# Kernel tuning notes

Hardware: AMD Instinct MI355X
Metric: run time of the kernel (lower is better)

## Reference

```python
import jax, jax.numpy as jnp
import numpy as np

# dims: batch, d_features(m), n_subsets, sub_size(k=ceil(m/n)), heads, d_k, d_v, conv kernel, d_out
B, M, N, K, H, DK, DV, KER, D = 512, 4096, 64, 64, 8, 32, 4, 3, 4096
DOUT_PER = D // N  # d_out_per_subset = 64
EPS_LN = 1e-5      # torch nn.LayerNorm default eps


def setup_inputs() -> dict:
    key = jax.random.key(0)
    ks = jax.random.split(key, 8)
    s = 0.02  # xavier-like scale
    return {
        "features": jax.random.normal(ks[0], (B, M), dtype=jnp.float32),
        # per-head permutation of the m feature indices (f_shuffle(m, h, seeds))
        "shuffled_index": jnp.argsort(jax.random.uniform(ks[1], (H, M)), axis=1).astype(jnp.int32),
        "gamma": jnp.ones((M,), jnp.float32),
        "beta": jnp.zeros((M,), jnp.float32),
        "W_q": (jax.random.normal(ks[2], (H * DK, K)) * s).astype(jnp.float32),   # Linear(k, h*d_k)
        "W_k": (jax.random.normal(ks[3], (H, DK, K)) * s).astype(jnp.float32),    # grouped Conv1d(h, h*d_k, kernel=k, stride=k)
        "W_v1": (jax.random.normal(ks[4], (H, DV, KER)) * s).astype(jnp.float32), # grouped Conv1d(h, h*d_v, kernel)
        "W_v2": (jax.random.normal(ks[5], (H, DV)) * s).astype(jnp.float32),      # grouped Conv1d(h*d_v, h, 1)
        "W_fc": (jax.random.normal(ks[6], (DOUT_PER, H * K)) * s).astype(jnp.float32),
    }


def reference(features, shuffled_index, gamma, beta, W_q, W_k, W_v1, W_v2, W_fc):
    b = features.shape[0]
    # LayerNorm over m (query path only)
    mu = features.mean(-1, keepdims=True)
    var = ((features - mu) ** 2).mean(-1, keepdims=True)
    q_in = (features - mu) / jnp.sqrt(var + EPS_LN) * gamma + beta

    # shuffled gather: [b, H, M]  (k*n == m here so k_pad/q_pad are no-ops)
    sf = features[:, shuffled_index]

    # query: [b, n, k] -> Linear(k, h*d_k) -> [b, H, N, DK]
    q = jnp.einsum('bnk,ek->bne', q_in.reshape(b, N, K), W_q)
    q = q.reshape(b, N, H, DK).transpose(0, 2, 1, 3)

    # key: grouped conv kernel=stride=k == per-subset contraction -> [b, H, DK, N]
    kf = sf.reshape(b, H, N, K)
    key_ = jnp.einsum('bhnk,hdk->bhdn', kf, W_k)

    # value: [b, N, H, K], right-pad by KER-1, depthwise conv -> relu -> 1x1 conv -> +residual
    v = kf.transpose(0, 2, 1, 3)  # [b, N, H, K]
    vp = jnp.pad(v, ((0, 0), (0, 0), (0, 0), (0, KER - 1)))
    win = jnp.stack([vp[..., t:t + K] for t in range(KER)], axis=-1)  # [b,N,H,K,KER]
    v1 = jnp.einsum('bnhpt,hdt->bnhdp', win, W_v1)
    v2 = jnp.einsum('bnhdp,hd->bnhp', jax.nn.relu(v1), W_v2)
    v = (v2 + v).transpose(0, 2, 1, 3)  # [b, H, N, K]

    # scaled dot-product attention, temperature = sqrt(m)
    attn = jax.nn.softmax(jnp.einsum('bhqd,bhdk->bhqk', q, key_) / jnp.sqrt(jnp.float32(M)), axis=-1)
    out = jnp.einsum('bhqk,bhks->bhqs', attn, v)           # [b, H, N, K]
    out = out.transpose(0, 2, 1, 3).reshape(b, N, H * K)   # [b, N, H*K]
    out = jnp.einsum('bnf,of->bno', out, W_fc).reshape(b, N * DOUT_PER)
    return out, attn.reshape(b * H, N, N)
```

## Files before the change

### kernel.cpp

```cpp
#include <hip/hip_runtime.h>

typedef __bf16 v8bf __attribute__((ext_vector_type(8)));
typedef __bf16 v4bf __attribute__((ext_vector_type(4)));
typedef __bf16 v2bf __attribute__((ext_vector_type(2)));
typedef float  v4f  __attribute__((ext_vector_type(4)));

namespace {

constexpr int kB = 512, kM = 4096, kH = 8;

constexpr size_t WS_QIN = 0;
constexpr size_t WS_O   = (size_t)4 << 20;
constexpr size_t WS_WQ  = WS_O + (size_t)32768 * 512 * 2;
constexpr size_t WS_WK  = WS_WQ + 32768;
constexpr size_t WS_WFC = WS_WK + 32768;


__global__ __launch_bounds__(256) void k0_weights(
    const float* __restrict__ Wq, const float* __restrict__ Wk,
    const float* __restrict__ Wfc,
    __bf16* __restrict__ wq, __bf16* __restrict__ wk, __bf16* __restrict__ wfc) {
  int i = blockIdx.x * 256 + threadIdx.x;
  if (i < 16384) {
    int e = i >> 6, k = i & 63;
    int dst = ((e >> 4) * 2 + (k >> 5)) * 512 + (e & 15) * 32 + (k & 31);
    wq[dst] = (__bf16)(Wq[i] * 0.015625f);
  } else if (i < 32768) {
    int j = i - 16384;
    int e = j >> 6, k = j & 63;
    int dst = ((e >> 4) * 2 + (k >> 5)) * 512 + (e & 15) * 32 + (k & 31);
    wk[dst] = (__bf16)Wk[j];
  } else {
    int j = i - 32768;
    int o = j >> 9, f = j & 511;
    int dst = ((o >> 4) * 16 + (f >> 5)) * 512 + (o & 15) * 32 + (f & 31);
    wfc[dst] = (__bf16)Wfc[j];
  }
}

__global__ __launch_bounds__(256) void k1_ln(
    const float* __restrict__ feat, const float* __restrict__ gamma,
    const float* __restrict__ beta, __bf16* __restrict__ qin) {
  __shared__ float red[4];
  const int b = blockIdx.x, t = threadIdx.x, lane = t & 63, wv = t >> 6;
  const float* frow = feat + (size_t)b * kM;
  float xs[16];
  float s = 0.f;
#pragma unroll
  for (int j = 0; j < 16; ++j) { float x = frow[t + j * 256]; xs[j] = x; s += x; }
#pragma unroll
  for (int o = 32; o > 0; o >>= 1) s += __shfl_xor(s, o);
  if (lane == 0) red[wv] = s;
  __syncthreads();
  const float mu = (red[0] + red[1] + red[2] + red[3]) * (1.f / kM);
  float v = 0.f;
#pragma unroll
  for (int j = 0; j < 16; ++j) { float d = xs[j] - mu; v += d * d; }
#pragma unroll
  for (int o = 32; o > 0; o >>= 1) v += __shfl_xor(v, o);
  __syncthreads();
  if (lane == 0) red[wv] = v;
  __syncthreads();
  const float var  = (red[0] + red[1] + red[2] + red[3]) * (1.f / kM);
  const float rstd = rsqrtf(var + 1e-5f);
#pragma unroll
  for (int j = 0; j < 16; ++j) {
    int m = t + j * 256;
    int n = m >> 6, k = m & 63;
    int dst = ((n >> 4) * 2 + (k >> 5)) * 512 + (n & 15) * 32 + (k & 31);
    qin[(size_t)b * kM + dst] = (__bf16)((xs[j] - mu) * rstd * gamma[m] + beta[m]);
  }
}

__global__ __launch_bounds__(256, 4) void k2_attn(
    const float* __restrict__ feat, const int* __restrict__ sidx,
    const __bf16* __restrict__ qin, const __bf16* __restrict__ wq,
    const __bf16* __restrict__ wk, const float* __restrict__ Wv1,
    const float* __restrict__ Wv2, __bf16* __restrict__ o_ws,
    float* __restrict__ out) {
  __shared__ __align__(16) __bf16 smem[18432];
  __bf16* s_feat = smem;
  __bf16* s_kf   = smem + 4096;
  __bf16* s_q    = smem + 8704;
  __bf16* s_K    = smem + 11264;
  __bf16* s_vT   = smem + 13824;
  __bf16* s_sc   = smem + 4096;

  const int b = blockIdx.x, h = blockIdx.y;
  const int t = threadIdx.x, w = t >> 6, lid = t & 63;
  const int quad = lid >> 4, l16 = lid & 15;

  const float*  frow  = feat + (size_t)b * kM;
  const int*    idxh  = sidx + h * kM;
  const __bf16* qin_b = qin + (size_t)b * kM;
  float* attn_out = out + (size_t)kB * kM + ((size_t)(b * kH + h)) * 4096;

  int idxr[16];
#pragma unroll
  for (int j = 0; j < 16; ++j) idxr[j] = idxh[t + j * 256];

  {
    const float4* frow4 = reinterpret_cast<const float4*>(frow);
#pragma unroll
    for (int j = 0; j < 4; ++j) {
      int i4 = t + j * 256;
      float4 f = frow4[i4];
      v4bf o4;
      o4[0] = (__bf16)f.x; o4[1] = (__bf16)f.y; o4[2] = (__bf16)f.z; o4[3] = (__bf16)f.w;
      *(v4bf*)(s_feat + 4 * i4) = o4;
    }
  }

  if (t < 64) {
    v8bf z = {};
    *(v8bf*)(s_kf + t * 72 + 64) = z;
  }

  v4f dq0 = {0.f, 0.f, 0.f, 0.f}, dq1 = {0.f, 0.f, 0.f, 0.f};
#pragma unroll
  for (int kt = 0; kt < 2; ++kt) {
    v8bf a  = *(const v8bf*)(qin_b + (2 * w + kt) * 512 + l16 * 32 + 8 * quad);
    v8bf b0 = *(const v8bf*)(wq + (size_t)(4 * h + kt) * 512 + l16 * 32 + 8 * quad);
    v8bf b1 = *(const v8bf*)(wq + (size_t)(4 * h + 2 + kt) * 512 + l16 * 32 + 8 * quad);
    dq0 = __builtin_amdgcn_mfma_f32_16x16x32_bf16(a, b0, dq0, 0, 0, 0);
    dq1 = __builtin_amdgcn_mfma_f32_16x16x32_bf16(a, b1, dq1, 0, 0, 0);
  }
#pragma unroll
  for (int r = 0; r < 4; ++r) {
    s_q[(16 * w + 4 * quad + r) * 40 + l16]      = (__bf16)dq0[r];
    s_q[(16 * w + 4 * quad + r) * 40 + 16 + l16] = (__bf16)dq1[r];
  }

  __syncthreads();

#pragma unroll
  for (int j = 0; j < 16; ++j) {
    int i = t + j * 256;
    s_kf[(i >> 6) * 72 + (i & 63)] = s_feat[idxr[j]];
  }

  __syncthreads();

  {
    v4f dk0 = {0.f, 0.f, 0.f, 0.f}, dk1 = {0.f, 0.f, 0.f, 0.f};
#pragma unroll
    for (int kt = 0; kt < 2; ++kt) {
      v8bf a  = *(const v8bf*)(s_kf + (16 * w + l16) * 72 + 32 * kt + 8 * quad);
      v8bf b0 = *(const v8bf*)(wk + (size_t)(4 * h + kt) * 512 + l16 * 32 + 8 * quad);
      v8bf b1 = *(const v8bf*)(wk + (size_t)(4 * h + 2 + kt) * 512 + l16 * 32 + 8 * quad);
      dk0 = __builtin_amdgcn_mfma_f32_16x16x32_bf16(a, b0, dk0, 0, 0, 0);
      dk1 = __builtin_amdgcn_mfma_f32_16x16x32_bf16(a, b1, dk1, 0, 0, 0);
    }
#pragma unroll
    for (int r = 0; r < 4; ++r) {
      s_K[(16 * w + 4 * quad + r) * 40 + l16]      = (__bf16)dk0[r];
      s_K[(16 * w + 4 * quad + r) * 40 + 16 + l16] = (__bf16)dk1[r];
    }
  }

  {
    const int n = t & 63, p0 = (t >> 6) * 16;
    float w1[4][3], w2[4];
#pragma unroll
    for (int d = 0; d < 4; ++d) {
#pragma unroll
      for (int c = 0; c < 3; ++c) w1[d][c] = Wv1[(h * 4 + d) * 3 + c];
      w2[d] = Wv2[h * 4 + d];
    }
    v8bf xa = *(const v8bf*)(s_kf + n * 72 + p0);
    v8bf xb = *(const v8bf*)(s_kf + n * 72 + p0 + 8);
    v2bf xc = *(const v2bf*)(s_kf + n * 72 + p0 + 16);
    float x[18];
#pragma unroll
    for (int c = 0; c < 8; ++c) { x[c] = (float)xa[c]; x[c + 8] = (float)xb[c]; }
    x[16] = (float)xc[0]; x[17] = (float)xc[1];
#pragma unroll
    for (int pp = 0; pp < 16; ++pp) {
      float acc = x[pp];
#pragma unroll
      for (int d = 0; d < 4; ++d) {
        float v1 = fmaf(x[pp + 2], w1[d][2], fmaf(x[pp + 1], w1[d][1], x[pp] * w1[d][0]));
        acc = fmaf(fmaxf(v1, 0.f), w2[d], acc);
      }
      s_vT[(p0 + pp) * 72 + n] = (__bf16)acc;
    }
  }

  __syncthreads();

  {
    v4f ds[4] = {{0.f, 0.f, 0.f, 0.f}, {0.f, 0.f, 0.f, 0.f},
                 {0.f, 0.f, 0.f, 0.f}, {0.f, 0.f, 0.f, 0.f}};
    v8bf a = *(const v8bf*)(s_q + (16 * w + l16) * 40 + 8 * quad);
#pragma unroll
    for (int nt = 0; nt < 4; ++nt) {
      v8bf bb = *(const v8bf*)(s_K + (16 * nt + l16) * 40 + 8 * quad);
      ds[nt] = __builtin_amdgcn_mfma_f32_16x16x32_bf16(a, bb, ds[nt], 0, 0, 0);
    }
#pragma unroll
    for (int nt = 0; nt < 4; ++nt)
#pragma unroll
      for (int r = 0; r < 4; ++r)
        s_sc[(16 * w + 4 * quad + r) * 72 + 16 * nt + l16] = (__bf16)ds[nt][r];
  }

#pragma unroll
  for (int rr = 0; rr < 4; ++rr) {
    const int row = 16 * w + 4 * rr + quad;
    v4bf pv = *(const v4bf*)(s_sc + row * 72 + 4 * l16);
    float e0 = (float)pv[0], e1 = (float)pv[1], e2 = (float)pv[2], e3 = (float)pv[3];
    float mx = fmaxf(fmaxf(e0, e1), fmaxf(e2, e3));
#pragma unroll
    for (int mk = 8; mk > 0; mk >>= 1) mx = fmaxf(mx, __shfl_xor(mx, mk));
    e0 = __expf(e0 - mx); e1 = __expf(e1 - mx);
    e2 = __expf(e2 - mx); e3 = __expf(e3 - mx);
    float ssum = e0 + e1 + e2 + e3;
#pragma unroll
    for (int mk = 8; mk > 0; mk >>= 1) ssum += __shfl_xor(ssum, mk);
    const float inv = 1.0f / ssum;
    e0 *= inv; e1 *= inv; e2 *= inv; e3 *= inv;
    *(float4*)(attn_out + row * 64 + 4 * l16) = make_float4(e0, e1, e2, e3);
    v4bf st;
    st[0] = (__bf16)e0; st[1] = (__bf16)e1; st[2] = (__bf16)e2; st[3] = (__bf16)e3;
    *(v4bf*)(s_sc + row * 72 + 4 * l16) = st;
  }

  v4f dO[4] = {{0.f, 0.f, 0.f, 0.f}, {0.f, 0.f, 0.f, 0.f},
               {0.f, 0.f, 0.f, 0.f}, {0.f, 0.f, 0.f, 0.f}};
#pragma unroll
  for (int kt = 0; kt < 2; ++kt) {
    v8bf a = *(const v8bf*)(s_sc + (16 * w + l16) * 72 + 32 * kt + 8 * quad);
#pragma unroll
    for (int st = 0; st < 4; ++st) {
      v8bf bb = *(const v8bf*)(s_vT + (16 * st + l16) * 72 + 32 * kt + 8 * quad);
      dO[st] = __builtin_amdgcn_mfma_f32_16x16x32_bf16(a, bb, dO[st], 0, 0, 0);
    }
  }

  __bf16* obase = o_ws + ((size_t)(b * 4 + w) * 16 + h * 2) * 512;
#pragma unroll
  for (int st = 0; st < 4; ++st)
#pragma unroll
    for (int r = 0; r < 4; ++r)
      obase[(st >> 1) * 512 + (4 * quad + r) * 32 + (st & 1) * 16 + l16] = (__bf16)dO[st][r];
}

__global__ __launch_bounds__(256, 4) void k3_fc(
    const __bf16* __restrict__ o_ws, const __bf16* __restrict__ wfc,
    float* __restrict__ out) {
  const int t = threadIdx.x, w = t >> 6, lid = t & 63;
  const int quad = lid >> 4, l16 = lid & 15;
  const size_t row0 = (size_t)blockIdx.x * 64 + 16 * w;
  const __bf16* abase = o_ws + (size_t)(blockIdx.x * 4 + w) * 16 * 512;
  v4f d[4] = {{0.f, 0.f, 0.f, 0.f}, {0.f, 0.f, 0.f, 0.f},
              {0.f, 0.f, 0.f, 0.f}, {0.f, 0.f, 0.f, 0.f}};
#pragma unroll 4
  for (int kt = 0; kt < 16; ++kt) {
    v8bf a = *(const v8bf*)(abase + kt * 512 + l16 * 32 + 8 * quad);
#pragma unroll
    for (int nt = 0; nt < 4; ++nt) {
      v8bf bb = *(const v8bf*)(wfc + (size_t)(nt * 16 + kt) * 512 + l16 * 32 + 8 * quad);
      d[nt] = __builtin_amdgcn_mfma_f32_16x16x32_bf16(a, bb, d[nt], 0, 0, 0);
    }
  }
#pragma unroll
  for (int nt = 0; nt < 4; ++nt)
#pragma unroll
    for (int r = 0; r < 4; ++r)
      out[(row0 + 4 * quad + r) * 64 + 16 * nt + l16] = d[nt][r];
}

}

extern "C" void kernel_launch(void* const* d_in, const int* in_sizes, int n_in,
                              void* d_out, int out_size, void* d_ws, size_t ws_size,
                              hipStream_t stream) {
  (void)in_sizes; (void)n_in; (void)out_size; (void)ws_size;
  const float* features = (const float*)d_in[0];
  const int*   sidx     = (const int*)d_in[1];
  const float* gamma    = (const float*)d_in[2];
  const float* beta     = (const float*)d_in[3];
  const float* Wq       = (const float*)d_in[4];
  const float* Wk       = (const float*)d_in[5];
  const float* Wv1      = (const float*)d_in[6];
  const float* Wv2      = (const float*)d_in[7];
  const float* Wfc      = (const float*)d_in[8];
  float* out = (float*)d_out;

  char* ws = (char*)d_ws;
  __bf16* ws_qin = (__bf16*)(ws + WS_QIN);
  __bf16* ws_o   = (__bf16*)(ws + WS_O);
  __bf16* ws_wq  = (__bf16*)(ws + WS_WQ);
  __bf16* ws_wk  = (__bf16*)(ws + WS_WK);
  __bf16* ws_wfc = (__bf16*)(ws + WS_WFC);

  hipLaunchKernelGGL(k0_weights, dim3(256), dim3(256), 0, stream,
                     Wq, Wk, Wfc, ws_wq, ws_wk, ws_wfc);
  hipLaunchKernelGGL(k1_ln, dim3(kB), dim3(256), 0, stream,
                     features, gamma, beta, ws_qin);
  hipLaunchKernelGGL(k2_attn, dim3(kB, kH), dim3(256), 0, stream,
                     features, sidx, ws_qin, ws_wq, ws_wk, Wv1, Wv2, ws_o, out);
  hipLaunchKernelGGL(k3_fc, dim3(kB), dim3(256), 0, stream,
                     ws_o, ws_wfc, out);
}
```

Baseline: 150.2 us.

## Fold W_q and W_k into a per-head combined matrix and keep softmax in registers

Precomputes a per-head 64x64 matrix Wq^T·Wk (with the temperature scale) in a small weight kernel. The attention kernel then computes qin·Wqk once and contracts it with the shuffled features, instead of building separate Q and K projections. Softmax now runs directly on the MFMA accumulators instead of going through an LDS round trip, and attention probabilities are written with nontemporal stores. LDS use drops, allowing occupancy to rise from 4 to 5 blocks, at the cost of an extra tiny serial precompute launch and a different bf16 rounding path.

```diff
diff --git a/kernel.cpp b/kernel.cpp
--- a/kernel.cpp
+++ b/kernel.cpp
@@ -11,30 +11,41 @@
 
 constexpr size_t WS_QIN = 0;
 constexpr size_t WS_O   = (size_t)4 << 20;
-constexpr size_t WS_WQ  = WS_O + (size_t)32768 * 512 * 2;
-constexpr size_t WS_WK  = WS_WQ + 32768;
-constexpr size_t WS_WFC = WS_WK + 32768;
-
-
-__global__ __launch_bounds__(256) void k0_weights(
+constexpr size_t WS_WFC = WS_O + (size_t)32768 * 512 * 2;
+constexpr size_t WS_WQK = WS_WFC + 65536;
+
+
+__global__ __launch_bounds__(256) void k0_wfc(
+    const float* __restrict__ Wfc, __bf16* __restrict__ wfc) {
+  int j = blockIdx.x * 256 + threadIdx.x;
+  int o = j >> 9, f = j & 511;
+  int dst = ((o >> 4) * 16 + (f >> 5)) * 512 + (o & 15) * 32 + (f & 31);
+  wfc[dst] = (__bf16)Wfc[j];
+}
+
+__global__ __launch_bounds__(256) void k0b_wqk(
     const float* __restrict__ Wq, const float* __restrict__ Wk,
-    const float* __restrict__ Wfc,
-    __bf16* __restrict__ wq, __bf16* __restrict__ wk, __bf16* __restrict__ wfc) {
-  int i = blockIdx.x * 256 + threadIdx.x;
-  if (i < 16384) {
-    int e = i >> 6, k = i & 63;
-    int dst = ((e >> 4) * 2 + (k >> 5)) * 512 + (e & 15) * 32 + (k & 31);
-    wq[dst] = (__bf16)(Wq[i] * 0.015625f);
-  } else if (i < 32768) {
-    int j = i - 16384;
-    int e = j >> 6, k = j & 63;
-    int dst = ((e >> 4) * 2 + (k >> 5)) * 512 + (e & 15) * 32 + (k & 31);
-    wk[dst] = (__bf16)Wk[j];
-  } else {
-    int j = i - 32768;
-    int o = j >> 9, f = j & 511;
-    int dst = ((o >> 4) * 16 + (f >> 5)) * 512 + (o & 15) * 32 + (f & 31);
-    wfc[dst] = (__bf16)Wfc[j];
+    __bf16* __restrict__ wqk) {
+  __shared__ float sq[2048], sk[2048];
+  const int h = blockIdx.x, t = threadIdx.x;
+#pragma unroll
+  for (int j = 0; j < 8; ++j) {
+    sq[t + j * 256] = Wq[h * 2048 + t + j * 256] * 0.015625f;
+    sk[t + j * 256] = Wk[h * 2048 + t + j * 256];
+  }
+  __syncthreads();
+  const int kp = t >> 2, kbase = (t & 3) * 16;
+  float wkr[32];
+#pragma unroll
+  for (int d = 0; d < 32; ++d) wkr[d] = sk[d * 64 + kp];
+#pragma unroll
+  for (int j = 0; j < 16; ++j) {
+    int k = kbase + j;
+    float acc = 0.f;
+#pragma unroll
+    for (int d = 0; d < 32; ++d) acc = fmaf(sq[d * 64 + k], wkr[d], acc);
+    int dst = h * 4096 + ((kp >> 4) * 2 + (k >> 5)) * 512 + (kp & 15) * 32 + (k & 31);
+    wqk[dst] = (__bf16)acc;
   }
 }
 
@@ -72,19 +83,15 @@
   }
 }
 
-__global__ __launch_bounds__(256, 4) void k2_attn(
+__global__ __launch_bounds__(256, 5) void k2_attn(
     const float* __restrict__ feat, const int* __restrict__ sidx,
-    const __bf16* __restrict__ qin, const __bf16* __restrict__ wq,
-    const __bf16* __restrict__ wk, const float* __restrict__ Wv1,
-    const float* __restrict__ Wv2, __bf16* __restrict__ o_ws,
-    float* __restrict__ out) {
-  __shared__ __align__(16) __bf16 smem[18432];
-  __bf16* s_feat = smem;
-  __bf16* s_kf   = smem + 4096;
-  __bf16* s_q    = smem + 8704;
-  __bf16* s_K    = smem + 11264;
-  __bf16* s_vT   = smem + 13824;
-  __bf16* s_sc   = smem + 4096;
+    const __bf16* __restrict__ qin, const __bf16* __restrict__ wqk,
+    const float* __restrict__ Wv1, const float* __restrict__ Wv2,
+    __bf16* __restrict__ o_ws, float* __restrict__ out) {
+  __shared__ __align__(16) __bf16 smem[13824];
+  __bf16* s_kf = smem;
+  __bf16* s_x  = smem + 4608;
+  __bf16* s_vT = smem + 9216;
 
   const int b = blockIdx.x, h = blockIdx.y;
   const int t = threadIdx.x, w = t >> 6, lid = t & 63;
@@ -93,6 +100,7 @@
   const float*  frow  = feat + (size_t)b * kM;
   const int*    idxh  = sidx + h * kM;
   const __bf16* qin_b = qin + (size_t)b * kM;
+  const __bf16* wqk_h = wqk + h * 4096;
   float* attn_out = out + (size_t)kB * kM + ((size_t)(b * kH + h)) * 4096;
 
   int idxr[16];
@@ -107,28 +115,13 @@
       float4 f = frow4[i4];
       v4bf o4;
       o4[0] = (__bf16)f.x; o4[1] = (__bf16)f.y; o4[2] = (__bf16)f.z; o4[3] = (__bf16)f.w;
-      *(v4bf*)(s_feat + 4 * i4) = o4;
+      *(v4bf*)(s_x + 4 * i4) = o4;
     }
   }
 
   if (t < 64) {
-    v8bf z = {};
-    *(v8bf*)(s_kf + t * 72 + 64) = z;
-  }
-
-  v4f dq0 = {0.f, 0.f, 0.f, 0.f}, dq1 = {0.f, 0.f, 0.f, 0.f};
-#pragma unroll
-  for (int kt = 0; kt < 2; ++kt) {
-    v8bf a  = *(const v8bf*)(qin_b + (2 * w + kt) * 512 + l16 * 32 + 8 * quad);
-    v8bf b0 = *(const v8bf*)(wq + (size_t)(4 * h + kt) * 512 + l16 * 32 + 8 * quad);
-    v8bf b1 = *(const v8bf*)(wq + (size_t)(4 * h + 2 + kt) * 512 + l16 * 32 + 8 * quad);
-    dq0 = __builtin_amdgcn_mfma_f32_16x16x32_bf16(a, b0, dq0, 0, 0, 0);
-    dq1 = __builtin_amdgcn_mfma_f32_16x16x32_bf16(a, b1, dq1, 0, 0, 0);
-  }
-#pragma unroll
-  for (int r = 0; r < 4; ++r) {
-    s_q[(16 * w + 4 * quad + r) * 40 + l16]      = (__bf16)dq0[r];
-    s_q[(16 * w + 4 * quad + r) * 40 + 16 + l16] = (__bf16)dq1[r];
+    v4bf z = {};
+    *(v4bf*)(s_kf + t * 72 + 64) = z;
   }
 
   __syncthreads();
@@ -136,27 +129,28 @@
 #pragma unroll
   for (int j = 0; j < 16; ++j) {
     int i = t + j * 256;
-    s_kf[(i >> 6) * 72 + (i & 63)] = s_feat[idxr[j]];
-  }
-
-  __syncthreads();
-
-  {
-    v4f dk0 = {0.f, 0.f, 0.f, 0.f}, dk1 = {0.f, 0.f, 0.f, 0.f};
-#pragma unroll
-    for (int kt = 0; kt < 2; ++kt) {
-      v8bf a  = *(const v8bf*)(s_kf + (16 * w + l16) * 72 + 32 * kt + 8 * quad);
-      v8bf b0 = *(const v8bf*)(wk + (size_t)(4 * h + kt) * 512 + l16 * 32 + 8 * quad);
-      v8bf b1 = *(const v8bf*)(wk + (size_t)(4 * h + 2 + kt) * 512 + l16 * 32 + 8 * quad);
-      dk0 = __builtin_amdgcn_mfma_f32_16x16x32_bf16(a, b0, dk0, 0, 0, 0);
-      dk1 = __builtin_amdgcn_mfma_f32_16x16x32_bf16(a, b1, dk1, 0, 0, 0);
-    }
-#pragma unroll
-    for (int r = 0; r < 4; ++r) {
-      s_K[(16 * w + 4 * quad + r) * 40 + l16]      = (__bf16)dk0[r];
-      s_K[(16 * w + 4 * quad + r) * 40 + 16 + l16] = (__bf16)dk1[r];
-    }
-  }
+    s_kf[(i >> 6) * 72 + (i & 63)] = s_x[idxr[j]];
+  }
+
+  v4f dT[4] = {{0.f, 0.f, 0.f, 0.f}, {0.f, 0.f, 0.f, 0.f},
+               {0.f, 0.f, 0.f, 0.f}, {0.f, 0.f, 0.f, 0.f}};
+#pragma unroll
+  for (int kt = 0; kt < 2; ++kt) {
+    v8bf a = *(const v8bf*)(qin_b + (2 * w + kt) * 512 + l16 * 32 + 8 * quad);
+#pragma unroll
+    for (int nt = 0; nt < 4; ++nt) {
+      v8bf bb = *(const v8bf*)(wqk_h + (nt * 2 + kt) * 512 + l16 * 32 + 8 * quad);
+      dT[nt] = __builtin_amdgcn_mfma_f32_16x16x32_bf16(a, bb, dT[nt], 0, 0, 0);
+    }
+  }
+
+  __syncthreads();
+
+#pragma unroll
+  for (int nt = 0; nt < 4; ++nt)
+#pragma unroll
+    for (int r = 0; r < 4; ++r)
+      s_x[(16 * w + 4 * quad + r) * 72 + 16 * nt + l16] = (__bf16)dT[nt][r];
 
   {
     const int n = t & 63, p0 = (t >> 6) * 16;
@@ -188,48 +182,54 @@
 
   __syncthreads();
 
-  {
-    v4f ds[4] = {{0.f, 0.f, 0.f, 0.f}, {0.f, 0.f, 0.f, 0.f},
-                 {0.f, 0.f, 0.f, 0.f}, {0.f, 0.f, 0.f, 0.f}};
-    v8bf a = *(const v8bf*)(s_q + (16 * w + l16) * 40 + 8 * quad);
+  v4f ds[4] = {{0.f, 0.f, 0.f, 0.f}, {0.f, 0.f, 0.f, 0.f},
+               {0.f, 0.f, 0.f, 0.f}, {0.f, 0.f, 0.f, 0.f}};
+#pragma unroll
+  for (int kt = 0; kt < 2; ++kt) {
+    v8bf a = *(const v8bf*)(s_x + (16 * w + l16) * 72 + 32 * kt + 8 * quad);
 #pragma unroll
     for (int nt = 0; nt < 4; ++nt) {
-      v8bf bb = *(const v8bf*)(s_K + (16 * nt + l16) * 40 + 8 * quad);
+      v8bf bb = *(const v8bf*)(s_kf + (16 * nt + l16) * 72 + 32 * kt + 8 * quad);
       ds[nt] = __builtin_amdgcn_mfma_f32_16x16x32_bf16(a, bb, ds[nt], 0, 0, 0);
     }
-#pragma unroll
-    for (int nt = 0; nt < 4; ++nt)
-#pragma unroll
-      for (int r = 0; r < 4; ++r)
-        s_sc[(16 * w + 4 * quad + r) * 72 + 16 * nt + l16] = (__bf16)ds[nt][r];
-  }
-
-#pragma unroll
-  for (int rr = 0; rr < 4; ++rr) {
-    const int row = 16 * w + 4 * rr + quad;
-    v4bf pv = *(const v4bf*)(s_sc + row * 72 + 4 * l16);
-    float e0 = (float)pv[0], e1 = (float)pv[1], e2 = (float)pv[2], e3 = (float)pv[3];
-    float mx = fmaxf(fmaxf(e0, e1), fmaxf(e2, e3));
+  }
+
+  v4bf attn_bf[4];
+#pragma unroll
+  for (int r = 0; r < 4; ++r) {
+    float v0 = ds[0][r], v1 = ds[1][r], v2 = ds[2][r], v3 = ds[3][r];
+    float mx = fmaxf(fmaxf(v0, v1), fmaxf(v2, v3));
 #pragma unroll
     for (int mk = 8; mk > 0; mk >>= 1) mx = fmaxf(mx, __shfl_xor(mx, mk));
-    e0 = __expf(e0 - mx); e1 = __expf(e1 - mx);
-    e2 = __expf(e2 - mx); e3 = __expf(e3 - mx);
-    float ssum = e0 + e1 + e2 + e3;
+    v0 = __expf(v0 - mx); v1 = __expf(v1 - mx);
+    v2 = __expf(v2 - mx); v3 = __expf(v3 - mx);
+    float ssum = v0 + v1 + v2 + v3;
 #pragma unroll
     for (int mk = 8; mk > 0; mk >>= 1) ssum += __shfl_xor(ssum, mk);
     const float inv = 1.0f / ssum;
-    e0 *= inv; e1 *= inv; e2 *= inv; e3 *= inv;
-    *(float4*)(attn_out + row * 64 + 4 * l16) = make_float4(e0, e1, e2, e3);
-    v4bf st;
-    st[0] = (__bf16)e0; st[1] = (__bf16)e1; st[2] = (__bf16)e2; st[3] = (__bf16)e3;
-    *(v4bf*)(s_sc + row * 72 + 4 * l16) = st;
-  }
+    v0 *= inv; v1 *= inv; v2 *= inv; v3 *= inv;
+    float* arow = attn_out + (16 * w + 4 * quad + r) * 64 + l16;
+    __builtin_nontemporal_store(v0, arow);
+    __builtin_nontemporal_store(v1, arow + 16);
+    __builtin_nontemporal_store(v2, arow + 32);
+    __builtin_nontemporal_store(v3, arow + 48);
+    attn_bf[r][0] = (__bf16)v0; attn_bf[r][1] = (__bf16)v1;
+    attn_bf[r][2] = (__bf16)v2; attn_bf[r][3] = (__bf16)v3;
+  }
+
+  __syncthreads();
+
+#pragma unroll
+  for (int r = 0; r < 4; ++r)
+#pragma unroll
+    for (int nt = 0; nt < 4; ++nt)
+      s_kf[(16 * w + 4 * quad + r) * 72 + 16 * nt + l16] = attn_bf[r][nt];
 
   v4f dO[4] = {{0.f, 0.f, 0.f, 0.f}, {0.f, 0.f, 0.f, 0.f},
                {0.f, 0.f, 0.f, 0.f}, {0.f, 0.f, 0.f, 0.f}};
 #pragma unroll
   for (int kt = 0; kt < 2; ++kt) {
-    v8bf a = *(const v8bf*)(s_sc + (16 * w + l16) * 72 + 32 * kt + 8 * quad);
+    v8bf a = *(const v8bf*)(s_kf + (16 * w + l16) * 72 + 32 * kt + 8 * quad);
 #pragma unroll
     for (int st = 0; st < 4; ++st) {
       v8bf bb = *(const v8bf*)(s_vT + (16 * st + l16) * 72 + 32 * kt + 8 * quad);
@@ -290,16 +290,15 @@
   char* ws = (char*)d_ws;
   __bf16* ws_qin = (__bf16*)(ws + WS_QIN);
   __bf16* ws_o   = (__bf16*)(ws + WS_O);
-  __bf16* ws_wq  = (__bf16*)(ws + WS_WQ);
-  __bf16* ws_wk  = (__bf16*)(ws + WS_WK);
   __bf16* ws_wfc = (__bf16*)(ws + WS_WFC);
-
-  hipLaunchKernelGGL(k0_weights, dim3(256), dim3(256), 0, stream,
-                     Wq, Wk, Wfc, ws_wq, ws_wk, ws_wfc);
+  __bf16* ws_wqk = (__bf16*)(ws + WS_WQK);
+
+  hipLaunchKernelGGL(k0_wfc, dim3(128), dim3(256), 0, stream, Wfc, ws_wfc);
+  hipLaunchKernelGGL(k0b_wqk, dim3(kH), dim3(256), 0, stream, Wq, Wk, ws_wqk);
   hipLaunchKernelGGL(k1_ln, dim3(kB), dim3(256), 0, stream,
                      features, gamma, beta, ws_qin);
   hipLaunchKernelGGL(k2_attn, dim3(kB, kH), dim3(256), 0, stream,
-                     features, sidx, ws_qin, ws_wq, ws_wk, Wv1, Wv2, ws_o, out);
+                     features, sidx, ws_qin, ws_wqk, Wv1, Wv2, ws_o, out);
   hipLaunchKernelGGL(k3_fc, dim3(kB), dim3(256), 0, stream,
                      ws_o, ws_wfc, out);
 }
```

New measurement: 156.3 us. 4.0% more time.
